# Kernel tuning notes

Measured on AMD Instinct MI355X. Metric: run time of the kernel, lower is better.

## Reference

```python
import jax, jax.numpy as jnp
import numpy as np
from jax import lax

B_, L_, D_ = 4, 3136, 256
DH, DS, DR = 256, 16, 16  # d_inner//2, d_state, dt_rank (ceil(256/16))


def _ln(x, g, b):
    m = x.mean(-1, keepdims=True)
    v = ((x - m) ** 2).mean(-1, keepdims=True)
    return (x - m) * lax.rsqrt(v + 1e-5) * g + b


def _dwconv_same(x, w):
    # x: (B, C, L), w: (C, 1, K) depthwise, padding='same', no bias
    return lax.conv_general_dilated(x, w, (1,), 'SAME',
        dimension_numbers=('NCH', 'OIH', 'NCH'), feature_group_count=x.shape[1])


def _selective_scan(u, delta, A, Bm, Cm, Dp, delta_bias):
    # u, delta: (b, d, l); A: (d, n); Bm, Cm: (b, n, l)
    delta = jax.nn.softplus(delta + delta_bias[None, :, None])
    dA = jnp.exp(jnp.einsum('bdl,dn->lbdn', delta, A))          # (l,b,d,n)
    dBu = jnp.einsum('bdl,bnl,bdl->lbdn', delta, Bm, u)          # (l,b,d,n)
    C_l = jnp.transpose(Cm, (2, 0, 1))                           # (l,b,n)
    h0 = jnp.zeros(dA.shape[1:], u.dtype)

    def step(h, inp):
        dA_t, dBu_t, C_t = inp
        h = dA_t * h + dBu_t
        return h, jnp.einsum('bdn,bn->bd', h, C_t)

    _, ys = lax.scan(step, h0, (dA, dBu, C_l))                   # ys: (l,b,d)
    return jnp.transpose(ys, (1, 2, 0)) + u * Dp[None, :, None]


def _mamba(x, in_proj_w, conv_x_w, conv_z_w, x_proj_w, dt_proj_w, dt_proj_b, A_log, Dp, out_proj_w):
    xz = jnp.einsum('bld,ed->bel', x, in_proj_w)                 # (b, 2*DH, l)
    xb, zb = xz[:, :DH], xz[:, DH:]
    xb = jax.nn.silu(_dwconv_same(xb, conv_x_w))
    zb = jax.nn.silu(_dwconv_same(zb, conv_z_w))
    x_dbl = jnp.einsum('bdl,ed->ble', xb, x_proj_w)              # (b, l, DR+2*DS)
    dt, Bm, Cm = x_dbl[..., :DR], x_dbl[..., DR:DR + DS], x_dbl[..., DR + DS:]
    delta = jnp.einsum('blr,dr->bdl', dt, dt_proj_w)             # (b, DH, l)
    Bm = jnp.transpose(Bm, (0, 2, 1))                            # (b, DS, l)
    Cm = jnp.transpose(Cm, (0, 2, 1))
    A = -jnp.exp(A_log)
    y = _selective_scan(xb, delta, A, Bm, Cm, Dp, dt_proj_b)     # (b, DH, l)
    y = jnp.concatenate([y, zb], axis=1)                         # (b, 2*DH, l)
    return jnp.einsum('bel,de->bld', y, out_proj_w)


def _block(x, ln1_g, ln1_b, ln2_g, ln2_b, in_proj_w, conv_x_w, conv_z_w,
           x_proj_w, dt_proj_w, dt_proj_b, A_log, Dp, out_proj_w,
           mlp_w1, mlp_b1, mlp_w2, mlp_b2):
    x = x + _mamba(_ln(x, ln1_g, ln1_b), in_proj_w, conv_x_w, conv_z_w,
                   x_proj_w, dt_proj_w, dt_proj_b, A_log, Dp, out_proj_w)
    h = _ln(x, ln2_g, ln2_b)
    h = jax.nn.gelu(jnp.einsum('bld,hd->blh', h, mlp_w1) + mlp_b1, approximate=False)
    return x + (jnp.einsum('blh,dh->bld', h, mlp_w2) + mlp_b2)


def setup_inputs() -> dict:
    key = jax.random.key(0)
    ks = jax.random.split(key, 12)
    f = lambda k, s, sc=0.02: jax.random.normal(k, s, dtype=jnp.float32) * sc
    dt = jnp.exp(jax.random.uniform(ks[9], (DH,), dtype=jnp.float32)
                 * (np.log(0.1) - np.log(0.001)) + np.log(0.001))
    dt = jnp.clip(dt, 1e-4)
    inv_dt = dt + jnp.log(-jnp.expm1(-dt))
    return {
        'x': jax.random.normal(ks[0], (B_, L_, D_), dtype=jnp.float32),
        'ln1_g': jnp.ones((D_,), jnp.float32), 'ln1_b': jnp.zeros((D_,), jnp.float32),
        'ln2_g': jnp.ones((D_,), jnp.float32), 'ln2_b': jnp.zeros((D_,), jnp.float32),
        'in_proj_w': f(ks[1], (2 * DH, D_)),
        'conv_x_w': f(ks[2], (DH, 1, 3), 0.1),
        'conv_z_w': f(ks[3], (DH, 1, 3), 0.1),
        'x_proj_w': f(ks[4], (DR + 2 * DS, DH)),
        'dt_proj_w': f(ks[5], (DH, DR), DR ** -0.5),
        'dt_proj_b': inv_dt,
        'A_log': jnp.log(jnp.tile(jnp.arange(1, DS + 1, dtype=jnp.float32)[None, :], (DH, 1))),
        'Dp': jnp.ones((DH,), jnp.float32),
        'out_proj_w': f(ks[6], (D_, 2 * DH)),
        'mlp_w1': f(ks[7], (4 * D_, D_)), 'mlp_b1': jnp.zeros((4 * D_,), jnp.float32),
        'mlp_w2': f(ks[8], (D_, 4 * D_)), 'mlp_b2': jnp.zeros((D_,), jnp.float32),
    }


def reference(x, ln1_g, ln1_b, ln2_g, ln2_b, in_proj_w, conv_x_w, conv_z_w,
              x_proj_w, dt_proj_w, dt_proj_b, A_log, Dp, out_proj_w,
              mlp_w1, mlp_b1, mlp_w2, mlp_b2):
    return _block(x, ln1_g, ln1_b, ln2_g, ln2_b, in_proj_w, conv_x_w, conv_z_w,
                  x_proj_w, dt_proj_w, dt_proj_b, A_log, Dp, out_proj_w,
                  mlp_w1, mlp_b1, mlp_w2, mlp_b2)
```

## Files before the change

kernel.cpp:

```cpp
#include <hip/hip_runtime.h>
#include <hip/hip_bf16.h>

#define B_ 4
#define L_ 3136
#define D_ 256
#define NCH 49
#define LCH 64
#define M_ (B_*L_)

__device__ __forceinline__ float bf2f(unsigned short u) {
    union { unsigned int i; float f; } v; v.i = ((unsigned int)u) << 16; return v.f;
}
__device__ __forceinline__ unsigned short f2bs(float f) {
    __hip_bfloat16 h = __float2bfloat16(f);
    return *(unsigned short*)&h;
}
__device__ __forceinline__ float ldw(const void* p, size_t i, bool bf) {
    return bf ? bf2f(((const unsigned short*)p)[i]) : ((const float*)p)[i];
}
__device__ __forceinline__ void cvt4(ushort4 a, float* o) {
    o[0] = bf2f(a.x); o[1] = bf2f(a.y); o[2] = bf2f(a.z); o[3] = bf2f(a.w);
}
__device__ __forceinline__ void cvt8g(const unsigned short* p, bool v, float* o) {
    if (v) {
        ushort4 a = *(const ushort4*)p;
        ushort4 b = *(const ushort4*)(p + 4);
        cvt4(a, o); cvt4(b, o + 4);
    } else {
        #pragma unroll
        for (int i = 0; i < 8; ++i) o[i] = 0.f;
    }
}
__device__ __forceinline__ float dpp_add_xor1(float x) {
    int m = __builtin_amdgcn_update_dpp(0, __float_as_int(x), 0xB1, 0xF, 0xF, true);
    return x + __int_as_float(m);
}
__device__ __forceinline__ float dpp_add_xor2(float x) {
    int m = __builtin_amdgcn_update_dpp(0, __float_as_int(x), 0x4E, 0xF, 0xF, true);
    return x + __int_as_float(m);
}

__global__ __launch_bounds__(256) void detect_kernel(
    const unsigned int* __restrict__ xw, int* __restrict__ flag)
{
    int t = threadIdx.x; int cnt = 0;
    for (int i = t; i < 2048; i += 256) {
        unsigned int lo = xw[i] & 0xFFFFu;
        unsigned int e = (lo >> 7) & 0xFFu;
        if (e >= 0x58u && e <= 0x97u) cnt++;
    }
    #pragma unroll
    for (int o = 32; o > 0; o >>= 1) cnt += __shfl_down(cnt, o);
    __shared__ int sred[4];
    if ((t & 63) == 0) sred[t >> 6] = cnt;
    __syncthreads();
    if (t == 0) flag[0] = (sred[0] + sred[1] + sred[2] + sred[3] > 1024) ? 1 : 0;
}

__global__ __launch_bounds__(256) void ln_kernel(
    const void* __restrict__ xin, int inmode,
    const void* __restrict__ g, const void* __restrict__ bsh,
    unsigned short* __restrict__ out, const int* __restrict__ flagp)
{
    const bool wbf = (*flagp != 0);
    const bool inbf = (inmode < 0) ? wbf : true;
    int row = blockIdx.x * 4 + (threadIdx.x >> 6);
    int lane = threadIdx.x & 63;
    size_t idx = (size_t)row * 256 + lane * 4;
    float v[4];
    if (inbf) {
        ushort4 a = *(const ushort4*)((const unsigned short*)xin + idx);
        cvt4(a, v);
    } else {
        float4 a = *(const float4*)((const float*)xin + idx);
        v[0] = a.x; v[1] = a.y; v[2] = a.z; v[3] = a.w;
    }
    float s = v[0] + v[1] + v[2] + v[3];
    float s2 = v[0]*v[0] + v[1]*v[1] + v[2]*v[2] + v[3]*v[3];
    #pragma unroll
    for (int o = 32; o > 0; o >>= 1) { s += __shfl_xor(s, o); s2 += __shfl_xor(s2, o); }
    float mean = s * (1.f / 256.f);
    float var  = s2 * (1.f / 256.f) - mean * mean;
    float rs = rsqrtf(var + 1e-5f);
    ushort4 o;
    o.x = f2bs((v[0] - mean) * rs * ldw(g, lane*4+0, wbf) + ldw(bsh, lane*4+0, wbf));
    o.y = f2bs((v[1] - mean) * rs * ldw(g, lane*4+1, wbf) + ldw(bsh, lane*4+1, wbf));
    o.z = f2bs((v[2] - mean) * rs * ldw(g, lane*4+2, wbf) + ldw(bsh, lane*4+2, wbf));
    o.w = f2bs((v[3] - mean) * rs * ldw(g, lane*4+3, wbf) + ldw(bsh, lane*4+3, wbf));
    *(ushort4*)(out + idx) = o;
}

enum { EPI_NONE = 0, EPI_SP = 1, EPI_RES = 2, EPI_GELU = 3, EPI_OUT = 4 };

typedef __attribute__((ext_vector_type(8))) short bf16x8;
typedef __attribute__((ext_vector_type(4))) float f32x4;

__device__ __forceinline__ void gload_lds16(const void* g, void* l) {
    __builtin_amdgcn_global_load_lds(
        (const __attribute__((address_space(1))) unsigned int*)g,
        (__attribute__((address_space(3))) unsigned int*)l, 16, 0, 0);
}

template<int EPI>
__global__ __launch_bounds__(256) void mgemm_kernel(
    const unsigned short* __restrict__ A, const unsigned short* __restrict__ A2, int Ksplit,
    const void* __restrict__ W, void* __restrict__ Cout,
    int N, int K, int lda, int ldc,
    const void* __restrict__ bias, const void* __restrict__ resb,
    const unsigned short* __restrict__ resf, const int* __restrict__ flagp)
{
    const bool wbf = (*flagp != 0);
    __shared__ unsigned short As[2][64][64];
    __shared__ unsigned short Ws[2][64][64];
    const int tid = threadIdx.x;

    const int nwg = gridDim.x * gridDim.y;
    int bid = blockIdx.y * gridDim.x + blockIdx.x;
    int wgid = ((nwg & 7) == 0) ? ((bid & 7) * (nwg >> 3) + (bid >> 3)) : bid;
    const int bx = wgid % gridDim.x;
    const int by = wgid / gridDim.x;
    const int bm = by * 64, bn = bx * 64;

    const int l = tid & 63, wid = tid >> 6;
    const int wr = wid >> 1, wc = wid & 1;
    const int lr = l & 15;
    const int lq = l >> 4;
    const int srow = tid >> 3;
    const int sblk = ((tid & 7) ^ (srow & 7)) * 8;
    const int dcol = (tid & 7) * 8;

    f32x4 acc[2][2] = {};
    const int NT = K >> 6;

    auto stage = [&](int buf, int k0s) {
        const unsigned short* Ab; int kc;
        if (k0s < Ksplit) { Ab = A;  kc = k0s; }
        else              { Ab = A2; kc = k0s - Ksplit; }
        gload_lds16(Ab + (size_t)(bm + srow) * lda + kc + sblk,      &As[buf][srow][dcol]);
        gload_lds16(Ab + (size_t)(bm + 32 + srow) * lda + kc + sblk, &As[buf][32 + srow][dcol]);
        if (wbf) {
            const unsigned short* Wb = (const unsigned short*)W;
            gload_lds16(Wb + (size_t)(bn + srow) * K + k0s + sblk,      &Ws[buf][srow][dcol]);
            gload_lds16(Wb + (size_t)(bn + 32 + srow) * K + k0s + sblk, &Ws[buf][32 + srow][dcol]);
        } else {
            const float* Wf = (const float*)W;
            #pragma unroll
            for (int h = 0; h < 2; ++h) {
                int row = h * 32 + srow;
                const float* p = Wf + (size_t)(bn + row) * K + k0s + (tid & 7) * 8;
                float4 w0 = *(const float4*)p;
                float4 w1 = *(const float4*)(p + 4);
                ushort4 o0, o1;
                o0.x = f2bs(w0.x); o0.y = f2bs(w0.y); o0.z = f2bs(w0.z); o0.w = f2bs(w0.w);
                o1.x = f2bs(w1.x); o1.y = f2bs(w1.y); o1.z = f2bs(w1.z); o1.w = f2bs(w1.w);
                *(ushort4*)&Ws[buf][row][sblk]     = o0;
                *(ushort4*)&Ws[buf][row][sblk + 4] = o1;
            }
        }
    };

    stage(0, 0);
    asm volatile("s_waitcnt vmcnt(0)" ::: "memory");
    __syncthreads();

    int cur = 0;
    for (int kt = 0; kt < NT; ++kt) {
        if (kt + 1 < NT) stage(cur ^ 1, (kt + 1) << 6);

        bf16x8 af[2][2], bfr[2][2];
        #pragma unroll
        for (int i = 0; i < 2; ++i) {
            #pragma unroll
            for (int ks = 0; ks < 2; ++ks) {
                int ca = ((ks * 4 + lq) ^ (lr & 7)) * 8;
                af[i][ks]  = *(const bf16x8*)&As[cur][wr * 32 + i * 16 + lr][ca];
                bfr[i][ks] = *(const bf16x8*)&Ws[cur][wc * 32 + i * 16 + lr][ca];
            }
        }
        #pragma unroll
        for (int ks = 0; ks < 2; ++ks)
            #pragma unroll
            for (int i = 0; i < 2; ++i)
                #pragma unroll
                for (int j = 0; j < 2; ++j)
                    acc[i][j] = __builtin_amdgcn_mfma_f32_16x16x32_bf16(af[i][ks], bfr[j][ks], acc[i][j], 0, 0, 0);

        if (kt + 1 < NT) {
            asm volatile("s_waitcnt vmcnt(0)" ::: "memory");
            __syncthreads();
            cur ^= 1;
        }
    }

    #pragma unroll
    for (int i = 0; i < 2; ++i) {
        #pragma unroll
        for (int j = 0; j < 2; ++j) {
            const int col = bn + wc * 32 + j * 16 + lr;
            #pragma unroll
            for (int e = 0; e < 4; ++e) {
                const int row = bm + wr * 32 + i * 16 + lq * 4 + e;
                float t = acc[i][j][e];
                if (EPI == EPI_RES) {
                    t += ldw(resb, (size_t)row * 256 + col, wbf);
                } else if (EPI == EPI_GELU) {
                    t += ldw(bias, col, wbf);
                    t = 0.5f * t * (1.f + erff(t * 0.70710678118654752f));
                } else if (EPI == EPI_OUT) {
                    t += ldw(bias, col, wbf) + bf2f(resf[(size_t)row * 256 + col]);
                }
                if (EPI == EPI_OUT && !wbf) {
                    ((float*)Cout)[(size_t)row * ldc + col] = t;
                } else {
                    ((unsigned short*)Cout)[(size_t)row * ldc + col] = f2bs(t);
                }
            }
        }
    }
}

__global__ __launch_bounds__(256) void xdt_kernel(
    const unsigned short* __restrict__ A, const void* __restrict__ Wx,
    const void* __restrict__ Wd, float* __restrict__ xdbl,
    unsigned short* __restrict__ delta, const void* __restrict__ bias,
    const int* __restrict__ flagp)
{
    const bool wbf = (*flagp != 0);
    __shared__ unsigned short As[2][64][64];
    __shared__ unsigned short Ws[2][64][64];
    __shared__ unsigned short Ahl[64][40];
    const int tid = threadIdx.x;
    const int bm = blockIdx.y * 64;

    const int l = tid & 63, wid = tid >> 6;
    const int wr = wid >> 1, wc = wid & 1;
    const int lr = l & 15, lq = l >> 4;
    const int srow = tid >> 3;
    const int sblk = ((tid & 7) ^ (srow & 7)) * 8;
    const int dcol = (tid & 7) * 8;

    {
        ushort4 zz4; zz4.x = 0; zz4.y = 0; zz4.z = 0; zz4.w = 0;
        int buf = tid >> 7, rr = 48 + ((tid >> 3) & 15), cc = (tid & 7) * 8;
        *(ushort4*)&Ws[buf][rr][cc] = zz4;
        *(ushort4*)&Ws[buf][rr][cc + 4] = zz4;
    }
    __syncthreads();

    f32x4 acc[2][2] = {};

    auto stage = [&](int buf, int k0s) {
        gload_lds16(A + (size_t)(bm + srow) * 256 + k0s + sblk,      &As[buf][srow][dcol]);
        gload_lds16(A + (size_t)(bm + 32 + srow) * 256 + k0s + sblk, &As[buf][32 + srow][dcol]);
        if (wbf) {
            const unsigned short* Wb = (const unsigned short*)Wx;
            gload_lds16(Wb + (size_t)srow * 256 + k0s + sblk, &Ws[buf][srow][dcol]);
            if (srow < 16)
                gload_lds16(Wb + (size_t)(32 + srow) * 256 + k0s + sblk, &Ws[buf][32 + srow][dcol]);
        } else {
            const float* Wf = (const float*)Wx;
            #pragma unroll
            for (int h = 0; h < 2; ++h) {
                int row = h * 32 + srow;
                if (row < 48) {
                    const float* p = Wf + (size_t)row * 256 + k0s + (tid & 7) * 8;
                    float4 w0 = *(const float4*)p;
                    float4 w1 = *(const float4*)(p + 4);
                    ushort4 o0, o1;
                    o0.x = f2bs(w0.x); o0.y = f2bs(w0.y); o0.z = f2bs(w0.z); o0.w = f2bs(w0.w);
                    o1.x = f2bs(w1.x); o1.y = f2bs(w1.y); o1.z = f2bs(w1.z); o1.w = f2bs(w1.w);
                    *(ushort4*)&Ws[buf][row][sblk]     = o0;
                    *(ushort4*)&Ws[buf][row][sblk + 4] = o1;
                }
            }
        }
    };

    stage(0, 0);
    asm volatile("s_waitcnt vmcnt(0)" ::: "memory");
    __syncthreads();

    int cur = 0;
    for (int kt = 0; kt < 4; ++kt) {
        if (kt + 1 < 4) stage(cur ^ 1, (kt + 1) << 6);
        bf16x8 af[2][2], bfr[2][2];
        #pragma unroll
        for (int i = 0; i < 2; ++i) {
            #pragma unroll
            for (int ks = 0; ks < 2; ++ks) {
                int ca = ((ks * 4 + lq) ^ (lr & 7)) * 8;
                af[i][ks]  = *(const bf16x8*)&As[cur][wr * 32 + i * 16 + lr][ca];
                bfr[i][ks] = *(const bf16x8*)&Ws[cur][wc * 32 + i * 16 + lr][ca];
            }
        }
        #pragma unroll
        for (int ks = 0; ks < 2; ++ks)
            #pragma unroll
            for (int i = 0; i < 2; ++i)
                #pragma unroll
                for (int j = 0; j < 2; ++j)
                    acc[i][j] = __builtin_amdgcn_mfma_f32_16x16x32_bf16(af[i][ks], bfr[j][ks], acc[i][j], 0, 0, 0);
        if (kt + 1 < 4) {
            asm volatile("s_waitcnt vmcnt(0)" ::: "memory");
            __syncthreads();
            cur ^= 1;
        }
    }

    #pragma unroll
    for (int i = 0; i < 2; ++i) {
        #pragma unroll
        for (int j = 0; j < 2; ++j) {
            const int col = wc * 32 + j * 16 + lr;
            #pragma unroll
            for (int e = 0; e < 4; ++e) {
                const int row = wr * 32 + i * 16 + lq * 4 + e;
                float t = acc[i][j][e];
                if (col < 48) xdbl[(size_t)(bm + row) * 48 + col] = t;
                if (wc == 0 && j == 0) {
                    unsigned short hi = f2bs(t);
                    Ahl[row][lr]      = hi;
                    Ahl[row][16 + lr] = f2bs(t - bf2f(hi));
                }
            }
        }
    }
    __syncthreads();

    const int wcol = wid * 64;
    const int kc = (lq & 1) * 8;
    bf16x8 bf[4];
    #pragma unroll
    for (int j = 0; j < 4; ++j) {
        int nrow = wcol + j * 16 + lr;
        if (wbf) {
            bf[j] = *(const bf16x8*)((const unsigned short*)Wd + (size_t)nrow * 16 + kc);
        } else {
            const float* p = (const float*)Wd + (size_t)nrow * 16 + kc;
            float4 w0 = *(const float4*)p;
            float4 w1 = *(const float4*)(p + 4);
            union { bf16x8 v; unsigned short s[8]; } u8;
            u8.s[0] = f2bs(w0.x); u8.s[1] = f2bs(w0.y); u8.s[2] = f2bs(w0.z); u8.s[3] = f2bs(w0.w);
            u8.s[4] = f2bs(w1.x); u8.s[5] = f2bs(w1.y); u8.s[6] = f2bs(w1.z); u8.s[7] = f2bs(w1.w);
            bf[j] = u8.v;
        }
    }
    bf16x8 af2[4];
    #pragma unroll
    for (int i = 0; i < 4; ++i)
        af2[i] = *(const bf16x8*)&Ahl[i * 16 + lr][lq * 8];

    f32x4 acc2[4][4] = {};
    #pragma unroll
    for (int i = 0; i < 4; ++i)
        #pragma unroll
        for (int j = 0; j < 4; ++j)
            acc2[i][j] = __builtin_amdgcn_mfma_f32_16x16x32_bf16(af2[i], bf[j], acc2[i][j], 0, 0, 0);

    #pragma unroll
    for (int i = 0; i < 4; ++i) {
        #pragma unroll
        for (int j = 0; j < 4; ++j) {
            const int col = wcol + j * 16 + lr;
            #pragma unroll
            for (int e = 0; e < 4; ++e) {
                const int row = i * 16 + lq * 4 + e;
                float t = acc2[i][j][e] + ldw(bias, col, wbf);
                t = (t > 20.f) ? t : log1pf(__expf(t));
                delta[(size_t)(bm + row) * 256 + col] = f2bs(t);
            }
        }
    }
}

__global__ __launch_bounds__(256) void conv_silu_kernel(
    const unsigned short* __restrict__ xz,
    const void* __restrict__ wx, const void* __restrict__ wz,
    unsigned short* __restrict__ u, unsigned short* __restrict__ z,
    const int* __restrict__ flagp)
{
    const bool wbf = (*flagp != 0);
    int sub = threadIdx.x >> 5;
    int cb = (threadIdx.x & 31) * 8;
    int bl = blockIdx.x * 8 + sub;
    int l = bl % L_;
    const unsigned short* r = xz + (size_t)bl * 512;
    bool hasm = (l > 0), hasp = (l < L_ - 1);

    float wxa[24], wza[24];
    if (wbf) {
        const unsigned short* px = (const unsigned short*)wx + 3 * cb;
        const unsigned short* pz = (const unsigned short*)wz + 3 * cb;
        #pragma unroll
        for (int t = 0; t < 3; ++t) {
            cvt4(*(const ushort4*)(px + t * 8), &wxa[t * 8]);
            cvt4(*(const ushort4*)(px + t * 8 + 4), &wxa[t * 8 + 4]);
            cvt4(*(const ushort4*)(pz + t * 8), &wza[t * 8]);
            cvt4(*(const ushort4*)(pz + t * 8 + 4), &wza[t * 8 + 4]);
        }
    } else {
        const float* px = (const float*)wx + 3 * cb;
        const float* pz = (const float*)wz + 3 * cb;
        #pragma unroll
        for (int t = 0; t < 6; ++t) {
            *(float4*)&wxa[t * 4] = *(const float4*)(px + t * 4);
            *(float4*)&wza[t * 4] = *(const float4*)(pz + t * 4);
        }
    }

    float xm[8], xc[8], xp[8];
    cvt8g(r + cb - 512, hasm, xm);
    cvt8g(r + cb,       true, xc);
    cvt8g(r + cb + 512, hasp, xp);
    ushort4 o0, o1;
    {
        unsigned short* op = (unsigned short*)&o0;
        unsigned short* op1 = (unsigned short*)&o1;
        #pragma unroll
        for (int j = 0; j < 8; ++j) {
            float v = xm[j] * wxa[3 * j] + xc[j] * wxa[3 * j + 1] + xp[j] * wxa[3 * j + 2];
            v = v / (1.f + __expf(-v));
            if (j < 4) op[j] = f2bs(v); else op1[j - 4] = f2bs(v);
        }
    }
    *(ushort4*)(u + (size_t)bl * 256 + cb) = o0;
    *(ushort4*)(u + (size_t)bl * 256 + cb + 4) = o1;

    cvt8g(r + cb - 256,  hasm, xm);
    cvt8g(r + 256 + cb,  true, xc);
    cvt8g(r + 768 + cb,  hasp, xp);
    {
        unsigned short* op = (unsigned short*)&o0;
        unsigned short* op1 = (unsigned short*)&o1;
        #pragma unroll
        for (int j = 0; j < 8; ++j) {
            float v = xm[j] * wza[3 * j] + xc[j] * wza[3 * j + 1] + xp[j] * wza[3 * j + 2];
            v = v / (1.f + __expf(-v));
            if (j < 4) op[j] = f2bs(v); else op1[j - 4] = f2bs(v);
        }
    }
    *(ushort4*)(z + (size_t)bl * 256 + cb) = o0;
    *(ushort4*)(z + (size_t)bl * 256 + cb + 4) = o1;
}

__global__ __launch_bounds__(256) void scan_a_kernel(
    const unsigned short* __restrict__ delta, const unsigned short* __restrict__ u,
    const float* __restrict__ xdbl, const void* __restrict__ A_log,
    float* __restrict__ hend, float* __restrict__ dsum, const int* __restrict__ flagp)
{
    const bool wbf = (*flagp != 0);
    int blk = blockIdx.x;
    int b = blk / (NCH * 16);
    int rem = blk % (NCH * 16);
    int c = rem / 16, db = rem % 16;

    __shared__ unsigned int sduT[16][68];
    __shared__ float sBT[16][68];

    const unsigned short* dp = delta + (size_t)b * L_ * 256;
    const unsigned short* up = u     + (size_t)b * L_ * 256;
    const float* xd = xdbl + (size_t)b * L_ * 48;

    int r = threadIdx.x >> 2, q = (threadIdx.x & 3) * 4;
    int lrow = c * 64 + r;
    {
        ushort4 dv = *(const ushort4*)(dp + (size_t)lrow * 256 + db * 16 + q);
        ushort4 uv = *(const ushort4*)(up + (size_t)lrow * 256 + db * 16 + q);
        sduT[q + 0][r] = (unsigned)dv.x | ((unsigned)uv.x << 16);
        sduT[q + 1][r] = (unsigned)dv.y | ((unsigned)uv.y << 16);
        sduT[q + 2][r] = (unsigned)dv.z | ((unsigned)uv.z << 16);
        sduT[q + 3][r] = (unsigned)dv.w | ((unsigned)uv.w << 16);
        float4 Bv = *(const float4*)(xd + (size_t)lrow * 48 + 16 + q);
        sBT[q + 0][r] = Bv.x; sBT[q + 1][r] = Bv.y;
        sBT[q + 2][r] = Bv.z; sBT[q + 3][r] = Bv.w;
    }
    __syncthreads();

    int g = threadIdx.x >> 4, n = threadIdx.x & 15;
    int d = db * 16 + g;
    float An2 = -__expf(ldw(A_log, d * 16 + n, wbf)) * 1.44269504088896f;
    float h = 0.f, s = 0.f;
    #pragma unroll 4
    for (int tb = 0; tb < 16; ++tb) {
        uint4 du4 = *(const uint4*)&sduT[g][tb * 4];
        float4 B4 = *(const float4*)&sBT[n][tb * 4];
        #pragma unroll
        for (int j = 0; j < 4; ++j) {
            unsigned du = (j == 0) ? du4.x : (j == 1) ? du4.y : (j == 2) ? du4.z : du4.w;
            float Bn = (j == 0) ? B4.x : (j == 1) ? B4.y : (j == 2) ? B4.z : B4.w;
            float ds = __uint_as_float(du << 16);
            float ut = __uint_as_float(du & 0xFFFF0000u);
            float e = exp2f(ds * An2);
            h = fmaf(e, h, ds * ut * Bn);
            s += ds;
        }
    }
    size_t pair = (size_t)b * 256 + d;
    hend[(pair * NCH + c) * 16 + n] = h;
    if (n == 0) dsum[pair * NCH + c] = s;
}

__global__ __launch_bounds__(64) void scan_b_kernel(
    const void* __restrict__ A_log, float* __restrict__ hend,
    const float* __restrict__ dsum, const int* __restrict__ flagp)
{
    const bool wbf = (*flagp != 0);
    int gid = blockIdx.x * 64 + threadIdx.x;
    int pair = gid >> 4, n = gid & 15;
    int d = pair & 255;
    float An = -__expf(ldw(A_log, d * 16 + n, wbf));
    float H = 0.f;
    #pragma unroll 1
    for (int c0 = 0; c0 < NCH; c0 += 7) {
        float he[7], dd[7];
        #pragma unroll
        for (int j = 0; j < 7; ++j) {
            he[j] = hend[((size_t)pair * NCH + c0 + j) * 16 + n];
            dd[j] = dsum[(size_t)pair * NCH + c0 + j];
        }
        #pragma unroll
        for (int j = 0; j < 7; ++j) {
            hend[((size_t)pair * NCH + c0 + j) * 16 + n] = H;
            H = __expf(An * dd[j]) * H + he[j];
        }
    }
}

__global__ __launch_bounds__(256) void scan_c_kernel(
    const unsigned short* __restrict__ delta, const unsigned short* __restrict__ u,
    const float* __restrict__ xdbl, const void* __restrict__ A_log,
    const void* __restrict__ Dp, const float* __restrict__ hinit,
    unsigned short* __restrict__ y, const int* __restrict__ flagp)
{
    const bool wbf = (*flagp != 0);
    int blk = blockIdx.x;
    int b = blk / (NCH * 16);
    int rem = blk % (NCH * 16);
    int c = rem / 16, db = rem % 16;

    __shared__ unsigned int sduT[16][68];
    __shared__ float sBCT[16][132];
    __shared__ float sypT[16][4][68];
    __shared__ unsigned short sy[64][16];

    const unsigned short* dp = delta + (size_t)b * L_ * 256;
    const unsigned short* up = u     + (size_t)b * L_ * 256;
    const float* xd = xdbl + (size_t)b * L_ * 48;

    int r = threadIdx.x >> 2, q = (threadIdx.x & 3) * 4;
    int lrow = c * 64 + r;
    {
        ushort4 dv = *(const ushort4*)(dp + (size_t)lrow * 256 + db * 16 + q);
        ushort4 uv = *(const ushort4*)(up + (size_t)lrow * 256 + db * 16 + q);
        sduT[q + 0][r] = (unsigned)dv.x | ((unsigned)uv.x << 16);
        sduT[q + 1][r] = (unsigned)dv.y | ((unsigned)uv.y << 16);
        sduT[q + 2][r] = (unsigned)dv.z | ((unsigned)uv.z << 16);
        sduT[q + 3][r] = (unsigned)dv.w | ((unsigned)uv.w << 16);
        float4 Bv = *(const float4*)(xd + (size_t)lrow * 48 + 16 + q);
        float4 Cv = *(const float4*)(xd + (size_t)lrow * 48 + 32 + q);
        float2 t0; t0.x = Bv.x; t0.y = Cv.x; *(float2*)&sBCT[q + 0][r * 2] = t0;
        float2 t1; t1.x = Bv.y; t1.y = Cv.y; *(float2*)&sBCT[q + 1][r * 2] = t1;
        float2 t2; t2.x = Bv.z; t2.y = Cv.z; *(float2*)&sBCT[q + 2][r * 2] = t2;
        float2 t3; t3.x = Bv.w; t3.y = Cv.w; *(float2*)&sBCT[q + 3][r * 2] = t3;
    }
    __syncthreads();

    int g = threadIdx.x >> 4, n = threadIdx.x & 15;
    int d = db * 16 + g;
    float An2 = -__expf(ldw(A_log, d * 16 + n, wbf)) * 1.44269504088896f;
    size_t pair = (size_t)b * 256 + d;
    float h = hinit[(pair * NCH + c) * 16 + n];
    const bool wlane = ((n & 3) == 0);
    const int p = n >> 2;
    #pragma unroll 4
    for (int tb = 0; tb < 16; ++tb) {
        uint4 du4 = *(const uint4*)&sduT[g][tb * 4];
        float4 bc01 = *(const float4*)&sBCT[n][tb * 8];
        float4 bc23 = *(const float4*)&sBCT[n][tb * 8 + 4];
        float yp4[4];
        #pragma unroll
        for (int j = 0; j < 4; ++j) {
            unsigned du = (j == 0) ? du4.x : (j == 1) ? du4.y : (j == 2) ? du4.z : du4.w;
            float Bn = (j == 0) ? bc01.x : (j == 1) ? bc01.z : (j == 2) ? bc23.x : bc23.z;
            float Cn = (j == 0) ? bc01.y : (j == 1) ? bc01.w : (j == 2) ? bc23.y : bc23.w;
            float ds = __uint_as_float(du << 16);
            float ut = __uint_as_float(du & 0xFFFF0000u);
            float e = exp2f(ds * An2);
            h = fmaf(e, h, ds * ut * Bn);
            float yp = h * Cn;
            yp = dpp_add_xor1(yp);
            yp = dpp_add_xor2(yp);
            yp4[j] = yp;
        }
        if (wlane) *(float4*)&sypT[g][p][tb * 4] = *(float4*)yp4;
    }
    __syncthreads();

    #pragma unroll
    for (int cc = 0; cc < 4; ++cc) {
        int cell = threadIdx.x + cc * 256;
        int t2 = cell >> 4, gg = cell & 15;
        float sum = sypT[gg][0][t2] + sypT[gg][1][t2] + sypT[gg][2][t2] + sypT[gg][3][t2];
        unsigned du = sduT[gg][t2];
        float ut = __uint_as_float(du & 0xFFFF0000u);
        float Dd = ldw(Dp, db * 16 + gg, wbf);
        sy[t2][gg] = f2bs(sum + ut * Dd);
    }
    __syncthreads();
    *(ushort4*)(y + ((size_t)b * L_ + c * 64 + r) * 256 + db * 16 + q) = *(ushort4*)&sy[r][q];
}

extern "C" void kernel_launch(void* const* d_in, const int* in_sizes, int n_in,
                              void* d_out, int out_size, void* d_ws, size_t ws_size,
                              hipStream_t stream) {
    const void* x         = d_in[0];
    const void* ln1_g     = d_in[1];
    const void* ln1_b     = d_in[2];
    const void* ln2_g     = d_in[3];
    const void* ln2_b     = d_in[4];
    const void* in_proj_w = d_in[5];
    const void* conv_x_w  = d_in[6];
    const void* conv_z_w  = d_in[7];
    const void* x_proj_w  = d_in[8];
    const void* dt_proj_w = d_in[9];
    const void* dt_proj_b = d_in[10];
    const void* A_log     = d_in[11];
    const void* Dp        = d_in[12];
    const void* out_proj_w= d_in[13];
    const void* mlp_w1    = d_in[14];
    const void* mlp_b1    = d_in[15];
    const void* mlp_w2    = d_in[16];
    const void* mlp_b2    = d_in[17];

    float* ws = (float*)d_ws;
    unsigned short* xz    = (unsigned short*)(ws);
    unsigned short* delta = (unsigned short*)(ws);
    unsigned short* yb    = (unsigned short*)(ws + 1605632);
    float*          xdbl  = ws + 3211264;
    float*          hend  = ws + 3813376;
    float*          dsum  = ws + 4616192;
    unsigned short* hmid  = (unsigned short*)(ws);
    unsigned short* ub    = (unsigned short*)(ws + 6422528);
    unsigned short* xres  = (unsigned short*)(ws + 6422528);
    unsigned short* xnb   = (unsigned short*)(ws + 8028160);
    int*            flag  = (int*)(ws + 9633792);

    dim3 blk(256);
    const int KNOSPLIT = 1 << 30;

    detect_kernel<<<1, blk, 0, stream>>>((const unsigned int*)x, flag);

    ln_kernel<<<M_ / 4, blk, 0, stream>>>(x, -1, ln1_g, ln1_b, xnb, flag);

    mgemm_kernel<EPI_NONE><<<dim3(8, 196), blk, 0, stream>>>(
        xnb, nullptr, KNOSPLIT, in_proj_w, xz, 512, 256, 256, 512, nullptr, nullptr, nullptr, flag);

    conv_silu_kernel<<<M_ / 8, blk, 0, stream>>>(xz, conv_x_w, conv_z_w, ub, xnb, flag);

    xdt_kernel<<<dim3(1, 196), blk, 0, stream>>>(
        ub, x_proj_w, dt_proj_w, xdbl, delta, dt_proj_b, flag);

    scan_a_kernel<<<B_ * NCH * 16, blk, 0, stream>>>(delta, ub, xdbl, A_log, hend, dsum, flag);
    scan_b_kernel<<<256, dim3(64), 0, stream>>>(A_log, hend, dsum, flag);
    scan_c_kernel<<<B_ * NCH * 16, blk, 0, stream>>>(delta, ub, xdbl, A_log, Dp, hend, yb, flag);

    mgemm_kernel<EPI_RES><<<dim3(4, 196), blk, 0, stream>>>(
        yb, xnb, 256, out_proj_w, xres, 256, 512, 256, 256, nullptr, x, nullptr, flag);

    ln_kernel<<<M_ / 4, blk, 0, stream>>>(xres, 1, ln2_g, ln2_b, xnb, flag);

    mgemm_kernel<EPI_GELU><<<dim3(16, 196), blk, 0, stream>>>(
        xnb, nullptr, KNOSPLIT, mlp_w1, hmid, 1024, 256, 256, 1024, mlp_b1, nullptr, nullptr, flag);

    mgemm_kernel<EPI_OUT><<<dim3(4, 196), blk, 0, stream>>>(
        hmid, nullptr, KNOSPLIT, mlp_w2, d_out, 256, 1024, 1024, 256, mlp_b2, nullptr, xres, flag);
}
```

Measured before the change: 317.5 us.

## Triple-buffer GEMM LDS pipeline and widen N tile for wide GEMMs

The GEMM kernel moves from double to triple-buffered LDS staging with partial vmcnt waits and raw s_barrier, so global-to-LDS loads run two tiles ahead of the MFMA work. A template parameter NB widens the N tile to 128 for the in_proj and MLP-up GEMMs, halving their grid and reusing each A tile across more output columns. The cost is more LDS per block (which can lower occupancy) and more accumulator registers. The fp32-weight path keeps a simpler single-lookahead loop.

```diff
diff --git a/kernel.cpp b/kernel.cpp
--- a/kernel.cpp
+++ b/kernel.cpp
@@ -101,7 +101,7 @@
         (__attribute__((address_space(3))) unsigned int*)l, 16, 0, 0);
 }
 
-template<int EPI>
+template<int EPI, int NB>
 __global__ __launch_bounds__(256) void mgemm_kernel(
     const unsigned short* __restrict__ A, const unsigned short* __restrict__ A2, int Ksplit,
     const void* __restrict__ W, void* __restrict__ Cout,
@@ -110,8 +110,10 @@
     const unsigned short* __restrict__ resf, const int* __restrict__ flagp)
 {
     const bool wbf = (*flagp != 0);
-    __shared__ unsigned short As[2][64][64];
-    __shared__ unsigned short Ws[2][64][64];
+    constexpr int BN = 64 * NB;
+    constexpr int J  = 2 * NB;
+    __shared__ unsigned short As[3][64][64];
+    __shared__ unsigned short Ws[3][BN][64];
     const int tid = threadIdx.x;
 
     const int nwg = gridDim.x * gridDim.y;
@@ -119,7 +121,7 @@
     int wgid = ((nwg & 7) == 0) ? ((bid & 7) * (nwg >> 3) + (bid >> 3)) : bid;
     const int bx = wgid % gridDim.x;
     const int by = wgid / gridDim.x;
-    const int bm = by * 64, bn = bx * 64;
+    const int bm = by * 64, bn = bx * BN;
 
     const int l = tid & 63, wid = tid >> 6;
     const int wr = wid >> 1, wc = wid & 1;
@@ -129,7 +131,7 @@
     const int sblk = ((tid & 7) ^ (srow & 7)) * 8;
     const int dcol = (tid & 7) * 8;
 
-    f32x4 acc[2][2] = {};
+    f32x4 acc[2][J] = {};
     const int NT = K >> 6;
 
     auto stage = [&](int buf, int k0s) {
@@ -140,12 +142,14 @@
         gload_lds16(Ab + (size_t)(bm + 32 + srow) * lda + kc + sblk, &As[buf][32 + srow][dcol]);
         if (wbf) {
             const unsigned short* Wb = (const unsigned short*)W;
-            gload_lds16(Wb + (size_t)(bn + srow) * K + k0s + sblk,      &Ws[buf][srow][dcol]);
-            gload_lds16(Wb + (size_t)(bn + 32 + srow) * K + k0s + sblk, &Ws[buf][32 + srow][dcol]);
+            #pragma unroll
+            for (int h = 0; h < 2 * NB; ++h)
+                gload_lds16(Wb + (size_t)(bn + h * 32 + srow) * K + k0s + sblk,
+                            &Ws[buf][h * 32 + srow][dcol]);
         } else {
             const float* Wf = (const float*)W;
             #pragma unroll
-            for (int h = 0; h < 2; ++h) {
+            for (int h = 0; h < 2 * NB; ++h) {
                 int row = h * 32 + srow;
                 const float* p = Wf + (size_t)(bn + row) * K + k0s + (tid & 7) * 8;
                 float4 w0 = *(const float4*)p;
@@ -159,44 +163,65 @@
         }
     };
 
-    stage(0, 0);
-    asm volatile("s_waitcnt vmcnt(0)" ::: "memory");
-    __syncthreads();
-
-    int cur = 0;
-    for (int kt = 0; kt < NT; ++kt) {
-        if (kt + 1 < NT) stage(cur ^ 1, (kt + 1) << 6);
-
-        bf16x8 af[2][2], bfr[2][2];
-        #pragma unroll
-        for (int i = 0; i < 2; ++i) {
+    auto compute = [&](int buf) {
+        bf16x8 af[2][2], bfr[J][2];
+        #pragma unroll
+        for (int i = 0; i < 2; ++i)
             #pragma unroll
             for (int ks = 0; ks < 2; ++ks) {
                 int ca = ((ks * 4 + lq) ^ (lr & 7)) * 8;
-                af[i][ks]  = *(const bf16x8*)&As[cur][wr * 32 + i * 16 + lr][ca];
-                bfr[i][ks] = *(const bf16x8*)&Ws[cur][wc * 32 + i * 16 + lr][ca];
-            }
-        }
+                af[i][ks] = *(const bf16x8*)&As[buf][wr * 32 + i * 16 + lr][ca];
+            }
+        #pragma unroll
+        for (int j = 0; j < J; ++j)
+            #pragma unroll
+            for (int ks = 0; ks < 2; ++ks) {
+                int ca = ((ks * 4 + lq) ^ (lr & 7)) * 8;
+                bfr[j][ks] = *(const bf16x8*)&Ws[buf][wc * (32 * NB) + j * 16 + lr][ca];
+            }
         #pragma unroll
         for (int ks = 0; ks < 2; ++ks)
             #pragma unroll
             for (int i = 0; i < 2; ++i)
                 #pragma unroll
-                for (int j = 0; j < 2; ++j)
+                for (int j = 0; j < J; ++j)
                     acc[i][j] = __builtin_amdgcn_mfma_f32_16x16x32_bf16(af[i][ks], bfr[j][ks], acc[i][j], 0, 0, 0);
-
-        if (kt + 1 < NT) {
-            asm volatile("s_waitcnt vmcnt(0)" ::: "memory");
-            __syncthreads();
-            cur ^= 1;
-        }
-    }
+    };
+
+    #define WAIT_LPS() do { \
+        if constexpr (NB == 1) asm volatile("s_waitcnt vmcnt(4)" ::: "memory"); \
+        else                   asm volatile("s_waitcnt vmcnt(6)" ::: "memory"); } while (0)
+
+    if (wbf) {
+        stage(0, 0);
+        if (NT > 1) { stage(1, 64); WAIT_LPS(); }
+        else        { asm volatile("s_waitcnt vmcnt(0)" ::: "memory"); }
+        __builtin_amdgcn_s_barrier();
+        for (int kt = 0; kt < NT; ++kt) {
+            if (kt + 2 < NT) stage((kt + 2) % 3, (kt + 2) << 6);
+            compute(kt % 3);
+            if (kt + 1 < NT) {
+                if (kt + 2 < NT) { WAIT_LPS(); }
+                else             { asm volatile("s_waitcnt vmcnt(0)" ::: "memory"); }
+                __builtin_amdgcn_s_barrier();
+            }
+        }
+    } else {
+        stage(0, 0);
+        __syncthreads();
+        for (int kt = 0; kt < NT; ++kt) {
+            if (kt + 1 < NT) stage((kt + 1) % 3, (kt + 1) << 6);
+            compute(kt % 3);
+            if (kt + 1 < NT) __syncthreads();
+        }
+    }
+    #undef WAIT_LPS
 
     #pragma unroll
     for (int i = 0; i < 2; ++i) {
         #pragma unroll
-        for (int j = 0; j < 2; ++j) {
-            const int col = bn + wc * 32 + j * 16 + lr;
+        for (int j = 0; j < J; ++j) {
+            const int col = bn + wc * (32 * NB) + j * 16 + lr;
             #pragma unroll
             for (int e = 0; e < 4; ++e) {
                 const int row = bm + wr * 32 + i * 16 + lq * 4 + e;
@@ -652,7 +677,7 @@
 
     ln_kernel<<<M_ / 4, blk, 0, stream>>>(x, -1, ln1_g, ln1_b, xnb, flag);
 
-    mgemm_kernel<EPI_NONE><<<dim3(8, 196), blk, 0, stream>>>(
+    mgemm_kernel<EPI_NONE, 2><<<dim3(4, 196), blk, 0, stream>>>(
         xnb, nullptr, KNOSPLIT, in_proj_w, xz, 512, 256, 256, 512, nullptr, nullptr, nullptr, flag);
 
     conv_silu_kernel<<<M_ / 8, blk, 0, stream>>>(xz, conv_x_w, conv_z_w, ub, xnb, flag);
@@ -664,14 +689,14 @@
     scan_b_kernel<<<256, dim3(64), 0, stream>>>(A_log, hend, dsum, flag);
     scan_c_kernel<<<B_ * NCH * 16, blk, 0, stream>>>(delta, ub, xdbl, A_log, Dp, hend, yb, flag);
 
-    mgemm_kernel<EPI_RES><<<dim3(4, 196), blk, 0, stream>>>(
+    mgemm_kernel<EPI_RES, 1><<<dim3(4, 196), blk, 0, stream>>>(
         yb, xnb, 256, out_proj_w, xres, 256, 512, 256, 256, nullptr, x, nullptr, flag);
 
     ln_kernel<<<M_ / 4, blk, 0, stream>>>(xres, 1, ln2_g, ln2_b, xnb, flag);
 
-    mgemm_kernel<EPI_GELU><<<dim3(16, 196), blk, 0, stream>>>(
+    mgemm_kernel<EPI_GELU, 2><<<dim3(8, 196), blk, 0, stream>>>(
         xnb, nullptr, KNOSPLIT, mlp_w1, hmid, 1024, 256, 256, 1024, mlp_b1, nullptr, nullptr, flag);
 
-    mgemm_kernel<EPI_OUT><<<dim3(4, 196), blk, 0, stream>>>(
+    mgemm_kernel<EPI_OUT, 1><<<dim3(4, 196), blk, 0, stream>>>(
         hmid, nullptr, KNOSPLIT, mlp_w2, d_out, 256, 1024, 1024, 256, mlp_b2, nullptr, xres, flag);
 }
```

Measured after the change: 431.6 us. 1.36x slower.
